# Kernel optimization log

Hardware: AMD Instinct MI355X
Metric: run time of the kernel (lower is better)

Reference implementation:

```python
import jax, jax.numpy as jnp
import numpy as np

D_MODEL = 1024
NUM_HEADS = 16
D_K = D_MODEL // NUM_HEADS
THETA = 10000.0
BATCH = 2
SEQ = 2048


def setup_inputs() -> dict:
    key = jax.random.key(0)
    ks = jax.random.split(key, 5)
    std = np.sqrt(2.0 / (D_MODEL + D_MODEL))
    return {
        "x": jax.random.normal(ks[0], (BATCH, SEQ, D_MODEL), dtype=jnp.float32),
        "Wq": jax.random.normal(ks[1], (D_MODEL, D_MODEL), dtype=jnp.float32) * std,
        "Wk": jax.random.normal(ks[2], (D_MODEL, D_MODEL), dtype=jnp.float32) * std,
        "Wv": jax.random.normal(ks[3], (D_MODEL, D_MODEL), dtype=jnp.float32) * std,
        "Wo": jax.random.normal(ks[4], (D_MODEL, D_MODEL), dtype=jnp.float32) * std,
        "token_positions": jnp.arange(SEQ, dtype=jnp.int64),
    }


def _apply_rope(t, cos, sin):
    # t: [B, H, S, D_K]; cos/sin: [S, D_K//2]
    # Block-diag 2x2 rotation on consecutive pairs (2k, 2k+1) == elementwise rotation.
    tr = t.reshape(*t.shape[:-1], D_K // 2, 2)
    t0, t1 = tr[..., 0], tr[..., 1]
    o0 = t0 * cos - t1 * sin
    o1 = t0 * sin + t1 * cos
    return jnp.stack([o0, o1], axis=-1).reshape(t.shape)


def reference(x, Wq, Wk, Wv, Wo, token_positions):
    B, S, _ = x.shape
    # projections: custom Linear does x @ W.T
    def split_heads(t):
        return t.reshape(B, S, NUM_HEADS, D_K).transpose(0, 2, 1, 3)  # [B,H,S,Dk]

    q = split_heads(x @ Wq.T)
    k = split_heads(x @ Wk.T)
    v = split_heads(x @ Wv.T)

    # RoPE angle table: theta_ik = pos / THETA**(2k/d_k)
    inv_freq = 1.0 / (THETA ** (2.0 * jnp.arange(D_K // 2, dtype=jnp.float32) / D_K))
    angles = token_positions.astype(jnp.float32)[:, None] * inv_freq[None, :]  # [S, Dk//2]
    cos, sin = jnp.cos(angles), jnp.sin(angles)

    q = _apply_rope(q, cos, sin)
    k = _apply_rope(k, cos, sin)

    scale = 1.0 / np.sqrt(D_K)
    scores = jnp.einsum("bhqd,bhkd->bhqk", q, k) * scale  # [B,H,S,S]
    causal = jnp.tril(jnp.ones((S, S), dtype=bool))
    scores = jnp.where(causal, scores, -jnp.inf)
    attn = jax.nn.softmax(scores, axis=-1)
    out = jnp.einsum("bhqk,bhkd->bhqd", attn, v)  # [B,H,S,Dk]
    out = out.transpose(0, 2, 1, 3).reshape(B, S, D_MODEL)
    return out @ Wo.T
```

## Files before the change

kernel.cpp:

```cpp
#include <hip/hip_runtime.h>
#include <hip/hip_bf16.h>
#include <cstdint>
#include <cstddef>

#define BATCH 2
#define SEQ   2048
#define DM    1024
#define NH    16
#define DK    64
#define LOG2E 1.4426950408889634f

typedef __attribute__((ext_vector_type(8)))  short short8;
typedef __attribute__((ext_vector_type(4)))  float f32x4;
typedef __attribute__((ext_vector_type(16))) float f32x16;
typedef __attribute__((ext_vector_type(4)))  int   i32x4;
typedef __attribute__((ext_vector_type(2)))  int   i32x2;

__device__ __forceinline__ void gload_lds16(const __hip_bfloat16* g, __hip_bfloat16* l) {
  __builtin_amdgcn_global_load_lds((const __attribute__((address_space(1))) void*)g,
                                   (__attribute__((address_space(3))) void*)l, 16, 0, 0);
}

__device__ __forceinline__ int cvtpk_bf16(float lo, float hi) {
  int r;
  asm("v_cvt_pk_bf16_f32 %0, %1, %2" : "=v"(r) : "v"(lo), "v"(hi));
  return r;
}

__device__ __forceinline__ float partner32(float x, int hi) {
  auto r = __builtin_amdgcn_permlane32_swap(__float_as_int(x), __float_as_int(x), false, false);
  return __int_as_float(hi ? r[0] : r[1]);
}

__global__ void cast_all(const float* __restrict__ x,  const float* __restrict__ Wq,
                         const float* __restrict__ Wk, const float* __restrict__ Wv,
                         const float* __restrict__ Wo, __hip_bfloat16* __restrict__ dst,
                         const int* __restrict__ pos,  float2* __restrict__ tbl) {
  const int NX = BATCH * SEQ * DM;
  int t = blockIdx.x * 256 + threadIdx.x;
  if (t < SEQ * 32) {
    int s = t >> 5, d2 = t & 31;
    float ang = (float)pos[s] * exp2f(-(float)d2 * 0.415241011860920f);
    float cv, sv;
    __sincosf(ang, &sv, &cv);
    tbl[t] = make_float2(cv, sv);
  }
  size_t i = (size_t)t * 4;
  const float* s;
  if (i < (size_t)NX) {
    s = x + i;
  } else {
    size_t j = i - NX;
    int wsel = (int)(j >> 20);
    size_t o = j & ((1u << 20) - 1);
    s = (wsel == 0 ? Wq : wsel == 1 ? Wk : wsel == 2 ? Wv : Wo) + o;
  }
  float4 v = *(const float4*)s;
  i32x2 pk;
  pk[0] = cvtpk_bf16(v.x, v.y);
  pk[1] = cvtpk_bf16(v.z, v.w);
  *(i32x2*)(dst + i) = pk;
}

template<bool F32OUT, bool VSPLIT>
__global__ __launch_bounds__(256)
void gemm_bt(const __hip_bfloat16* __restrict__ A,
             const __hip_bfloat16* __restrict__ Bw,
             void* __restrict__ Cv, __hip_bfloat16* __restrict__ vt,
             const float2* __restrict__ tbl,
             int M, int N, int K, int ldc) {
  __shared__ __hip_bfloat16 As[128 * 32];
  __shared__ __hip_bfloat16 Bs[128 * 32];
  const int tid  = threadIdx.x;
  const int lane = tid & 63;
  const int w    = tid >> 6;
  const int wr   = w >> 1, wc = w & 1;
  const int g    = lane >> 4;
  const int lr   = lane & 15;
  const int bm0  = blockIdx.y * 128;
  const int bn0  = blockIdx.x * 128;

  f32x4 acc[4][4] = {};

  const int strow = lane >> 2;
  const int stc   = lane & 3;
  for (int kt = 0; kt < K; kt += 32) {
    #pragma unroll
    for (int it = 0; it < 2; ++it) {
      int c   = w * 2 + it;
      int row = c * 16 + strow;
      int csrc = stc ^ (row & 3);
      gload_lds16(A  + (size_t)(bm0 + row) * K + kt + csrc * 8, As + row * 32 + stc * 8);
      gload_lds16(Bw + (size_t)(bn0 + row) * K + kt + csrc * 8, Bs + row * 32 + stc * 8);
    }
    __syncthreads();
    short8 a[4], b[4];
    #pragma unroll
    for (int m = 0; m < 4; ++m) {
      int row = wr * 64 + m * 16 + lr;
      a[m] = *(const short8*)(As + row * 32 + ((g ^ (row & 3)) << 3));
    }
    #pragma unroll
    for (int n = 0; n < 4; ++n) {
      int row = wc * 64 + n * 16 + lr;
      b[n] = *(const short8*)(Bs + row * 32 + ((g ^ (row & 3)) << 3));
    }
    #pragma unroll
    for (int m = 0; m < 4; ++m)
      #pragma unroll
      for (int n = 0; n < 4; ++n)
        acc[m][n] = __builtin_amdgcn_mfma_f32_16x16x32_bf16(a[m], b[n], acc[m][n], 0, 0, 0);
    __syncthreads();
  }

  if (VSPLIT && bn0 >= 2048) {
    #pragma unroll
    for (int m = 0; m < 4; ++m)
      #pragma unroll
      for (int n = 0; n < 4; ++n) {
        int nn = bn0 + wc * 64 + n * 16 + lr - 2048;
        int hd = nn >> 6, d = nn & 63;
        int m0 = bm0 + wr * 64 + m * 16 + g * 4;
        int bb = m0 >> 11, ss = m0 & 2047;
        i32x2 pk;
        pk[0] = cvtpk_bf16(acc[m][n][0], acc[m][n][1]);
        pk[1] = cvtpk_bf16(acc[m][n][2], acc[m][n][3]);
        *(i32x2*)(vt + ((size_t)(bb * NH + hd) * DK + d) * SEQ + ss) = pk;
      }
  } else if (VSPLIT) {
    const bool isQ = (bn0 < 1024);
    const float qsc = isQ ? 0.125f * LOG2E : 1.0f;
    #pragma unroll
    for (int m = 0; m < 4; ++m)
      #pragma unroll
      for (int n = 0; n < 4; ++n) {
        int col = bn0 + wc * 64 + n * 16 + lr;
        int d   = col & 63;
        int odd = d & 1, d2 = d >> 1;
        #pragma unroll
        for (int r = 0; r < 4; ++r) {
          int row = bm0 + wr * 64 + m * 16 + g * 4 + r;
          float own  = acc[m][n][r];
          float part = __shfl_xor(own, 1, 64);
          float2 cs  = tbl[(row & (SEQ - 1)) * 32 + d2];
          float val  = odd ? (part * cs.y + own * cs.x) : (own * cs.x - part * cs.y);
          ((__hip_bfloat16*)Cv)[(size_t)row * ldc + col] = __float2bfloat16(val * qsc);
        }
      }
  } else {
    #pragma unroll
    for (int m = 0; m < 4; ++m)
      #pragma unroll
      for (int n = 0; n < 4; ++n) {
        int col = bn0 + wc * 64 + n * 16 + lr;
        #pragma unroll
        for (int r = 0; r < 4; ++r) {
          int row = bm0 + wr * 64 + m * 16 + g * 4 + r;
          float v = acc[m][n][r];
          if (F32OUT) ((float*)Cv)[(size_t)row * ldc + col] = v;
          else        ((__hip_bfloat16*)Cv)[(size_t)row * ldc + col] = __float2bfloat16(v);
        }
      }
  }
}

__global__ __launch_bounds__(512)
void flash_attn(const __hip_bfloat16* __restrict__ qk,
                const __hip_bfloat16* __restrict__ vt,
                __hip_bfloat16* __restrict__ outb) {
  __shared__ __hip_bfloat16 Kls[2][64 * 64];
  __shared__ __hip_bfloat16 Vls[2][64 * 64];
  const int pi = blockIdx.x;
  const int NQB = SEQ / 128;
  const int qbh = NQB - 1 - pi, qbl = pi;
  const int hd = blockIdx.y, b = blockIdx.z;
  const int tid = threadIdx.x, lane = tid & 63, w = tid >> 6;
  const int wh = w & 3;
  const int qb_eff = (w < 4) ? qbh : qbl;
  const int hi = lane >> 5, ql = lane & 31;
  const int q0w = qb_eff * 128 + wh * 32;
  const int nt  = 2 * qbh + 2;
  const int tmaxw = 2 * qb_eff + (wh >> 1);

  const __hip_bfloat16* Qb = qk + (size_t)(b * SEQ) * 2048 + hd * DK;
  const __hip_bfloat16* Kg = qk + (size_t)(b * SEQ) * 2048 + 1024 + hd * DK;
  const __hip_bfloat16* Vg = vt + (size_t)(b * NH + hd) * DK * SEQ;

  short8 qf[4];
  #pragma unroll
  for (int c = 0; c < 4; ++c)
    qf[c] = *(const short8*)(Qb + (size_t)(q0w + ql) * 2048 + c * 16 + hi * 8);

  f32x16 o0 = {}, o1 = {};
  float m_run = -1e30f, l_run = 0.f;

  const int srow = tid >> 3;
  const int sc0  = (tid & 7) * 8;
  const int swz  = (srow & 7) << 3;

  short8 kr, vr;
  kr = *(const short8*)(Kg + (size_t)srow * 2048 + sc0);
  vr = *(const short8*)(Vg + (size_t)srow * SEQ + sc0);
  *(short8*)(&Kls[0][srow * 64 + (sc0 ^ swz)]) = kr;
  *(short8*)(&Vls[0][srow * 64 + (sc0 ^ swz)]) = vr;

  for (int t = 0; t < nt; ++t) {
    const int cur = t & 1;
    if (t + 1 < nt) {
      int r0 = (t + 1) * 64;
      kr = *(const short8*)(Kg + (size_t)(r0 + srow) * 2048 + sc0);
      vr = *(const short8*)(Vg + (size_t)srow * SEQ + r0 + sc0);
    }
    __syncthreads();

    if (t <= tmaxw) {
      f32x16 s0 = {}, s1 = {};
      __builtin_amdgcn_s_setprio(1);
      #pragma unroll
      for (int c = 0; c < 4; ++c) {
        int col = (c * 16 + hi * 8) ^ ((ql & 7) << 3);
        short8 ka = *(const short8*)(&Kls[cur][ql * 64 + col]);
        short8 kb = *(const short8*)(&Kls[cur][(32 + ql) * 64 + col]);
        s0 = __builtin_amdgcn_mfma_f32_32x32x16_bf16(ka, qf[c], s0, 0, 0, 0);
        s1 = __builtin_amdgcn_mfma_f32_32x32x16_bf16(kb, qf[c], s1, 0, 0, 0);
      }
      __builtin_amdgcn_s_setprio(0);

      if (t * 64 + 63 > q0w) {
        int qg = q0w + ql;
        #pragma unroll
        for (int r = 0; r < 16; ++r) {
          int krow = (r & 3) + 8 * (r >> 2) + 4 * hi;
          if (t * 64 + krow > qg)      s0[r] = -1e30f;
          if (t * 64 + 32 + krow > qg) s1[r] = -1e30f;
        }
      }

      float mx = s0[0];
      #pragma unroll
      for (int r = 1; r < 16; ++r) mx = fmaxf(mx, s0[r]);
      #pragma unroll
      for (int r = 0; r < 16; ++r) mx = fmaxf(mx, s1[r]);
      mx = fmaxf(mx, partner32(mx, hi));

      if (!__all(mx <= m_run + 8.f)) {
        float mn  = fmaxf(m_run, mx);
        float fac = __builtin_amdgcn_exp2f(m_run - mn);
        m_run = mn;
        l_run *= fac;
        #pragma unroll
        for (int r = 0; r < 16; ++r) { o0[r] *= fac; o1[r] *= fac; }
      }
      float sum = 0.f;
      #pragma unroll
      for (int r = 0; r < 16; ++r) { s0[r] = __builtin_amdgcn_exp2f(s0[r] - m_run); sum += s0[r]; }
      #pragma unroll
      for (int r = 0; r < 16; ++r) { s1[r] = __builtin_amdgcn_exp2f(s1[r] - m_run); sum += s1[r]; }
      sum += partner32(sum, hi);
      l_run += sum;

      short8 pf[4];
      #pragma unroll
      for (int kt = 0; kt < 2; ++kt) {
        const f32x16& sv = kt ? s1 : s0;
        #pragma unroll
        for (int u = 0; u < 2; ++u) {
          int wa0 = cvtpk_bf16(sv[8 * u + 0], sv[8 * u + 1]);
          int wa1 = cvtpk_bf16(sv[8 * u + 2], sv[8 * u + 3]);
          int wb0 = cvtpk_bf16(sv[8 * u + 4], sv[8 * u + 5]);
          int wb1 = cvtpk_bf16(sv[8 * u + 6], sv[8 * u + 7]);
          auto r0 = __builtin_amdgcn_permlane32_swap(wa0, wb0, false, false);
          auto r1 = __builtin_amdgcn_permlane32_swap(wa1, wb1, false, false);
          i32x4 fr; fr[0] = r0[0]; fr[1] = r1[0]; fr[2] = r0[1]; fr[3] = r1[1];
          pf[kt * 2 + u] = *(short8*)&fr;
        }
      }

      __builtin_amdgcn_s_setprio(1);
      #pragma unroll
      for (int cc = 0; cc < 4; ++cc) {
        int col = (cc * 16 + hi * 8) ^ ((ql & 7) << 3);
        short8 va = *(const short8*)(&Vls[cur][ql * 64 + col]);
        short8 vb = *(const short8*)(&Vls[cur][(32 + ql) * 64 + col]);
        o0 = __builtin_amdgcn_mfma_f32_32x32x16_bf16(va, pf[cc], o0, 0, 0, 0);
        o1 = __builtin_amdgcn_mfma_f32_32x32x16_bf16(vb, pf[cc], o1, 0, 0, 0);
      }
      __builtin_amdgcn_s_setprio(0);
    }

    if (t + 1 < nt) {
      const int nxt = cur ^ 1;
      *(short8*)(&Kls[nxt][srow * 64 + (sc0 ^ swz)]) = kr;
      *(short8*)(&Vls[nxt][srow * 64 + (sc0 ^ swz)]) = vr;
    }
  }

  float inv = 1.f / l_run;
  __hip_bfloat16* orow = outb + (size_t)(b * SEQ + q0w + ql) * DM + hd * DK;
  #pragma unroll
  for (int dt = 0; dt < 2; ++dt) {
    const f32x16& oa = dt ? o1 : o0;
    #pragma unroll
    for (int a = 0; a < 4; ++a) {
      int d0 = dt * 32 + a * 8 + hi * 4;
      i32x2 pk;
      pk[0] = cvtpk_bf16(oa[4 * a + 0] * inv, oa[4 * a + 1] * inv);
      pk[1] = cvtpk_bf16(oa[4 * a + 2] * inv, oa[4 * a + 3] * inv);
      *(i32x2*)(orow + d0) = pk;
    }
  }
}

extern "C" void kernel_launch(void* const* d_in, const int* in_sizes, int n_in,
                              void* d_out, int out_size, void* d_ws, size_t ws_size,
                              hipStream_t stream) {
  const float* x  = (const float*)d_in[0];
  const float* Wq = (const float*)d_in[1];
  const float* Wk = (const float*)d_in[2];
  const float* Wv = (const float*)d_in[3];
  const float* Wo = (const float*)d_in[4];
  const int*   tp = (const int*)d_in[5];
  float* out = (float*)d_out;

  char* ws = (char*)d_ws;
  __hip_bfloat16* xb    = (__hip_bfloat16*)(ws);
  __hip_bfloat16* wqkv  = (__hip_bfloat16*)(ws + (8u  << 20));
  __hip_bfloat16* wob   = (__hip_bfloat16*)(ws + (14u << 20));
  __hip_bfloat16* qkbuf = (__hip_bfloat16*)(ws + (16u << 20));
  __hip_bfloat16* vtbuf = (__hip_bfloat16*)(ws + (32u << 20));
  __hip_bfloat16* attnb = (__hip_bfloat16*)(ws + (40u << 20));
  float2*         tbl   = (float2*)(ws + (40u << 20));

  cast_all<<<8192, 256, 0, stream>>>(x, Wq, Wk, Wv, Wo, xb, tp, tbl);

  gemm_bt<false, true><<<dim3(3 * DM / 128, BATCH * SEQ / 128), 256, 0, stream>>>(
      xb, wqkv, (void*)qkbuf, vtbuf, tbl, BATCH * SEQ, 3 * DM, DM, 2048);

  flash_attn<<<dim3(SEQ / 256, NH, BATCH), 512, 0, stream>>>(qkbuf, vtbuf, attnb);

  gemm_bt<true, false><<<dim3(DM / 128, BATCH * SEQ / 128), 256, 0, stream>>>(
      attnb, wob, (void*)out, nullptr, nullptr, BATCH * SEQ, DM, DM, DM);
}
```

Before: 128.5 us.

## Use two-wave GEMM blocks with 64x128 warp tiles and DPP pair swap

Reworks the bf16 GEMM so each 128-thread block uses two waves, each computing a 64x128 sub-tile, doubling per-wave accumulator reuse of B fragments. Removes the LDS XOR swizzle for a plain row layout and replaces the xor-1 shuffle in the RoPE epilogue with a DPP quad permute. This is meant to cut LDS reads per MFMA and shuffle cost, but it raises register pressure and may reintroduce LDS bank conflicts and fewer waves per block.

```diff
diff --git a/kernel.cpp b/kernel.cpp
--- a/kernel.cpp
+++ b/kernel.cpp
@@ -25,6 +25,10 @@
   int r;
   asm("v_cvt_pk_bf16_f32 %0, %1, %2" : "=v"(r) : "v"(lo), "v"(hi));
   return r;
+}
+
+__device__ __forceinline__ float dpp_xor1(float x) {
+  return __int_as_float(__builtin_amdgcn_mov_dpp(__float_as_int(x), 0xB1, 0xF, 0xF, true));
 }
 
 __device__ __forceinline__ float partner32(float x, int hi) {
@@ -63,7 +67,7 @@
 }
 
 template<bool F32OUT, bool VSPLIT>
-__global__ __launch_bounds__(256)
+__global__ __launch_bounds__(128)
 void gemm_bt(const __hip_bfloat16* __restrict__ A,
              const __hip_bfloat16* __restrict__ Bw,
              void* __restrict__ Cv, __hip_bfloat16* __restrict__ vt,
@@ -74,41 +78,35 @@
   const int tid  = threadIdx.x;
   const int lane = tid & 63;
   const int w    = tid >> 6;
-  const int wr   = w >> 1, wc = w & 1;
   const int g    = lane >> 4;
   const int lr   = lane & 15;
   const int bm0  = blockIdx.y * 128;
   const int bn0  = blockIdx.x * 128;
 
-  f32x4 acc[4][4] = {};
-
-  const int strow = lane >> 2;
-  const int stc   = lane & 3;
+  f32x4 acc[4][8] = {};
+
+  const int strow = tid >> 2;
+  const int stcol = (tid & 3) * 8;
+
   for (int kt = 0; kt < K; kt += 32) {
     #pragma unroll
-    for (int it = 0; it < 2; ++it) {
-      int c   = w * 2 + it;
-      int row = c * 16 + strow;
-      int csrc = stc ^ (row & 3);
-      gload_lds16(A  + (size_t)(bm0 + row) * K + kt + csrc * 8, As + row * 32 + stc * 8);
-      gload_lds16(Bw + (size_t)(bn0 + row) * K + kt + csrc * 8, Bs + row * 32 + stc * 8);
+    for (int p = 0; p < 4; ++p) {
+      int row = p * 32 + strow;
+      gload_lds16(A  + (size_t)(bm0 + row) * K + kt + stcol, As + row * 32 + stcol);
+      gload_lds16(Bw + (size_t)(bn0 + row) * K + kt + stcol, Bs + row * 32 + stcol);
     }
     __syncthreads();
-    short8 a[4], b[4];
-    #pragma unroll
-    for (int m = 0; m < 4; ++m) {
-      int row = wr * 64 + m * 16 + lr;
-      a[m] = *(const short8*)(As + row * 32 + ((g ^ (row & 3)) << 3));
-    }
-    #pragma unroll
-    for (int n = 0; n < 4; ++n) {
-      int row = wc * 64 + n * 16 + lr;
-      b[n] = *(const short8*)(Bs + row * 32 + ((g ^ (row & 3)) << 3));
-    }
-    #pragma unroll
-    for (int m = 0; m < 4; ++m)
-      #pragma unroll
-      for (int n = 0; n < 4; ++n)
+    short8 a[4], b[8];
+    #pragma unroll
+    for (int m = 0; m < 4; ++m)
+      a[m] = *(const short8*)(As + (w * 64 + m * 16 + lr) * 32 + g * 8);
+    #pragma unroll
+    for (int n = 0; n < 8; ++n)
+      b[n] = *(const short8*)(Bs + (n * 16 + lr) * 32 + g * 8);
+    #pragma unroll
+    for (int m = 0; m < 4; ++m)
+      #pragma unroll
+      for (int n = 0; n < 8; ++n)
         acc[m][n] = __builtin_amdgcn_mfma_f32_16x16x32_bf16(a[m], b[n], acc[m][n], 0, 0, 0);
     __syncthreads();
   }
@@ -117,10 +115,10 @@
     #pragma unroll
     for (int m = 0; m < 4; ++m)
       #pragma unroll
-      for (int n = 0; n < 4; ++n) {
-        int nn = bn0 + wc * 64 + n * 16 + lr - 2048;
+      for (int n = 0; n < 8; ++n) {
+        int nn = bn0 + n * 16 + lr - 2048;
         int hd = nn >> 6, d = nn & 63;
-        int m0 = bm0 + wr * 64 + m * 16 + g * 4;
+        int m0 = bm0 + w * 64 + m * 16 + g * 4;
         int bb = m0 >> 11, ss = m0 & 2047;
         i32x2 pk;
         pk[0] = cvtpk_bf16(acc[m][n][0], acc[m][n][1]);
@@ -133,15 +131,15 @@
     #pragma unroll
     for (int m = 0; m < 4; ++m)
       #pragma unroll
-      for (int n = 0; n < 4; ++n) {
-        int col = bn0 + wc * 64 + n * 16 + lr;
+      for (int n = 0; n < 8; ++n) {
+        int col = bn0 + n * 16 + lr;
         int d   = col & 63;
         int odd = d & 1, d2 = d >> 1;
         #pragma unroll
         for (int r = 0; r < 4; ++r) {
-          int row = bm0 + wr * 64 + m * 16 + g * 4 + r;
+          int row = bm0 + w * 64 + m * 16 + g * 4 + r;
           float own  = acc[m][n][r];
-          float part = __shfl_xor(own, 1, 64);
+          float part = dpp_xor1(own);
           float2 cs  = tbl[(row & (SEQ - 1)) * 32 + d2];
           float val  = odd ? (part * cs.y + own * cs.x) : (own * cs.x - part * cs.y);
           ((__hip_bfloat16*)Cv)[(size_t)row * ldc + col] = __float2bfloat16(val * qsc);
@@ -151,11 +149,11 @@
     #pragma unroll
     for (int m = 0; m < 4; ++m)
       #pragma unroll
-      for (int n = 0; n < 4; ++n) {
-        int col = bn0 + wc * 64 + n * 16 + lr;
+      for (int n = 0; n < 8; ++n) {
+        int col = bn0 + n * 16 + lr;
         #pragma unroll
         for (int r = 0; r < 4; ++r) {
-          int row = bm0 + wr * 64 + m * 16 + g * 4 + r;
+          int row = bm0 + w * 64 + m * 16 + g * 4 + r;
           float v = acc[m][n][r];
           if (F32OUT) ((float*)Cv)[(size_t)row * ldc + col] = v;
           else        ((__hip_bfloat16*)Cv)[(size_t)row * ldc + col] = __float2bfloat16(v);
@@ -333,11 +331,11 @@
 
   cast_all<<<8192, 256, 0, stream>>>(x, Wq, Wk, Wv, Wo, xb, tp, tbl);
 
-  gemm_bt<false, true><<<dim3(3 * DM / 128, BATCH * SEQ / 128), 256, 0, stream>>>(
+  gemm_bt<false, true><<<dim3(3 * DM / 128, BATCH * SEQ / 128), 128, 0, stream>>>(
       xb, wqkv, (void*)qkbuf, vtbuf, tbl, BATCH * SEQ, 3 * DM, DM, 2048);
 
   flash_attn<<<dim3(SEQ / 256, NH, BATCH), 512, 0, stream>>>(qkbuf, vtbuf, attnb);
 
-  gemm_bt<true, false><<<dim3(DM / 128, BATCH * SEQ / 128), 256, 0, stream>>>(
+  gemm_bt<true, false><<<dim3(DM / 128, BATCH * SEQ / 128), 128, 0, stream>>>(
       attnb, wob, (void*)out, nullptr, nullptr, BATCH * SEQ, DM, DM, DM);
 }
```

Result: slower. 157.9 us (+22.9%).

## Double-buffer GEMM LDS tiles, remap blocks across XCDs, split RoPE into separate kernel

Applied to the files above, without the earlier changes.

The projection GEMM now keeps two LDS buffers so the next K-tile's global-to-LDS load is issued while the current tile feeds MFMA, and it remaps block IDs so consecutive tiles land on the same XCD group. The XOR swizzle on LDS rows is removed, which may bring back bank conflicts on the short8 reads. The RoPE rotation and Q scaling move out of the GEMM epilogue into a separate vectorized kernel, which adds an extra read and write pass over the Q/K buffer and one more launch in exchange for a simpler GEMM epilogue.

```diff
diff --git a/kernel.cpp b/kernel.cpp
--- a/kernel.cpp
+++ b/kernel.cpp
@@ -25,6 +25,10 @@
   int r;
   asm("v_cvt_pk_bf16_f32 %0, %1, %2" : "=v"(r) : "v"(lo), "v"(hi));
   return r;
+}
+
+__device__ __forceinline__ float bf2f(short v) {
+  return __int_as_float(((int)(unsigned short)v) << 16);
 }
 
 __device__ __forceinline__ float partner32(float x, int hi) {
@@ -67,50 +71,58 @@
 void gemm_bt(const __hip_bfloat16* __restrict__ A,
              const __hip_bfloat16* __restrict__ Bw,
              void* __restrict__ Cv, __hip_bfloat16* __restrict__ vt,
-             const float2* __restrict__ tbl,
              int M, int N, int K, int ldc) {
-  __shared__ __hip_bfloat16 As[128 * 32];
-  __shared__ __hip_bfloat16 Bs[128 * 32];
+  __shared__ __hip_bfloat16 As[2][128 * 32];
+  __shared__ __hip_bfloat16 Bs[2][128 * 32];
   const int tid  = threadIdx.x;
   const int lane = tid & 63;
   const int w    = tid >> 6;
   const int wr   = w >> 1, wc = w & 1;
   const int g    = lane >> 4;
   const int lr   = lane & 15;
-  const int bm0  = blockIdx.y * 128;
-  const int bn0  = blockIdx.x * 128;
+
+  const int nwg = gridDim.x * gridDim.y;
+  const int bid = blockIdx.y * gridDim.x + blockIdx.x;
+  const int cpx = nwg >> 3;
+  const int sbid = (bid & 7) * cpx + (bid >> 3);
+  const int bx = sbid % gridDim.x, by = sbid / gridDim.x;
+  const int bm0  = by * 128;
+  const int bn0  = bx * 128;
 
   f32x4 acc[4][4] = {};
 
   const int strow = lane >> 2;
-  const int stc   = lane & 3;
-  for (int kt = 0; kt < K; kt += 32) {
+  const int stcol = (lane & 3) * 8;
+
+  auto STAGE = [&](int buf, int kt) {
     #pragma unroll
     for (int it = 0; it < 2; ++it) {
-      int c   = w * 2 + it;
-      int row = c * 16 + strow;
-      int csrc = stc ^ (row & 3);
-      gload_lds16(A  + (size_t)(bm0 + row) * K + kt + csrc * 8, As + row * 32 + stc * 8);
-      gload_lds16(Bw + (size_t)(bn0 + row) * K + kt + csrc * 8, Bs + row * 32 + stc * 8);
-    }
-    __syncthreads();
+      int row = (w * 2 + it) * 16 + strow;
+      gload_lds16(A  + (size_t)(bm0 + row) * K + kt + stcol, &As[buf][row * 32 + stcol]);
+      gload_lds16(Bw + (size_t)(bn0 + row) * K + kt + stcol, &Bs[buf][row * 32 + stcol]);
+    }
+  };
+
+  STAGE(0, 0);
+  __syncthreads();
+  int cur = 0;
+  const int nk = K / 32;
+  for (int ki = 0; ki < nk; ++ki) {
+    if (ki + 1 < nk) STAGE(cur ^ 1, (ki + 1) * 32);
     short8 a[4], b[4];
     #pragma unroll
-    for (int m = 0; m < 4; ++m) {
-      int row = wr * 64 + m * 16 + lr;
-      a[m] = *(const short8*)(As + row * 32 + ((g ^ (row & 3)) << 3));
-    }
-    #pragma unroll
-    for (int n = 0; n < 4; ++n) {
-      int row = wc * 64 + n * 16 + lr;
-      b[n] = *(const short8*)(Bs + row * 32 + ((g ^ (row & 3)) << 3));
-    }
+    for (int m = 0; m < 4; ++m)
+      a[m] = *(const short8*)(&As[cur][(wr * 64 + m * 16 + lr) * 32 + g * 8]);
+    #pragma unroll
+    for (int n = 0; n < 4; ++n)
+      b[n] = *(const short8*)(&Bs[cur][(wc * 64 + n * 16 + lr) * 32 + g * 8]);
     #pragma unroll
     for (int m = 0; m < 4; ++m)
       #pragma unroll
       for (int n = 0; n < 4; ++n)
         acc[m][n] = __builtin_amdgcn_mfma_f32_16x16x32_bf16(a[m], b[n], acc[m][n], 0, 0, 0);
     __syncthreads();
+    cur ^= 1;
   }
 
   if (VSPLIT && bn0 >= 2048) {
@@ -127,26 +139,6 @@
         pk[1] = cvtpk_bf16(acc[m][n][2], acc[m][n][3]);
         *(i32x2*)(vt + ((size_t)(bb * NH + hd) * DK + d) * SEQ + ss) = pk;
       }
-  } else if (VSPLIT) {
-    const bool isQ = (bn0 < 1024);
-    const float qsc = isQ ? 0.125f * LOG2E : 1.0f;
-    #pragma unroll
-    for (int m = 0; m < 4; ++m)
-      #pragma unroll
-      for (int n = 0; n < 4; ++n) {
-        int col = bn0 + wc * 64 + n * 16 + lr;
-        int d   = col & 63;
-        int odd = d & 1, d2 = d >> 1;
-        #pragma unroll
-        for (int r = 0; r < 4; ++r) {
-          int row = bm0 + wr * 64 + m * 16 + g * 4 + r;
-          float own  = acc[m][n][r];
-          float part = __shfl_xor(own, 1, 64);
-          float2 cs  = tbl[(row & (SEQ - 1)) * 32 + d2];
-          float val  = odd ? (part * cs.y + own * cs.x) : (own * cs.x - part * cs.y);
-          ((__hip_bfloat16*)Cv)[(size_t)row * ldc + col] = __float2bfloat16(val * qsc);
-        }
-      }
   } else {
     #pragma unroll
     for (int m = 0; m < 4; ++m)
@@ -162,6 +154,29 @@
         }
       }
   }
+}
+
+__global__ void rope_vec(__hip_bfloat16* __restrict__ qk, const float2* __restrict__ tbl) {
+  int idx = blockIdx.x * 256 + threadIdx.x;
+  int row = idx >> 7;
+  int hg  = idx & 127;
+  int h   = hg >> 3, gg = hg & 7;
+  const float QS = 0.125f * LOG2E;
+  size_t base = (size_t)row * 2048 + h * 64 + gg * 8;
+  const float2* tp = tbl + (row & (SEQ - 1)) * 32 + gg * 4;
+  short8 q = *(const short8*)(qk + base);
+  short8 k = *(const short8*)(qk + base + 1024);
+  i32x4 qo, ko;
+  #pragma unroll
+  for (int j = 0; j < 4; ++j) {
+    float2 cs = tp[j];
+    float q0 = bf2f(q[2 * j]), q1 = bf2f(q[2 * j + 1]);
+    float k0 = bf2f(k[2 * j]), k1 = bf2f(k[2 * j + 1]);
+    qo[j] = cvtpk_bf16((q0 * cs.x - q1 * cs.y) * QS, (q0 * cs.y + q1 * cs.x) * QS);
+    ko[j] = cvtpk_bf16(k0 * cs.x - k1 * cs.y,        k0 * cs.y + k1 * cs.x);
+  }
+  *(i32x4*)(qk + base)        = qo;
+  *(i32x4*)(qk + base + 1024) = ko;
 }
 
 __global__ __launch_bounds__(512)
@@ -334,10 +349,12 @@
   cast_all<<<8192, 256, 0, stream>>>(x, Wq, Wk, Wv, Wo, xb, tp, tbl);
 
   gemm_bt<false, true><<<dim3(3 * DM / 128, BATCH * SEQ / 128), 256, 0, stream>>>(
-      xb, wqkv, (void*)qkbuf, vtbuf, tbl, BATCH * SEQ, 3 * DM, DM, 2048);
+      xb, wqkv, (void*)qkbuf, vtbuf, BATCH * SEQ, 3 * DM, DM, 2048);
+
+  rope_vec<<<(BATCH * SEQ * NH * 8) / 256, 256, 0, stream>>>(qkbuf, tbl);
 
   flash_attn<<<dim3(SEQ / 256, NH, BATCH), 512, 0, stream>>>(qkbuf, vtbuf, attnb);
 
   gemm_bt<true, false><<<dim3(DM / 128, BATCH * SEQ / 128), 256, 0, stream>>>(
-      attnb, wob, (void*)out, nullptr, nullptr, BATCH * SEQ, DM, DM, DM);
-}
+      attnb, wob, (void*)out, nullptr, BATCH * SEQ, DM, DM, DM);
+}
```

Result: faster. 116.8 us (-9.1%).
